# Kernel optimization log

Hardware: AMD Instinct MI355X
Metric: run time of the kernel (lower is better)

## Reference

```python
import jax, jax.numpy as jnp
import numpy as np

NV, NC, E, H, L = 100_000, 420_000, 630_000, 128, 8
ALPHA, THETA = 0.1, 0.5


def _seg_mean(msgs, dst, n_dst):
    # mean aggregation over destination segments (PyG SAGEConv default)
    s = jax.ops.segment_sum(msgs, dst, num_segments=n_dst)
    cnt = jax.ops.segment_sum(jnp.ones((dst.shape[0], 1), msgs.dtype), dst, num_segments=n_dst)
    return s / jnp.maximum(cnt, 1.0)


def _sage(x_src, x_dst, src, dst, n_dst, Wl, bl, Wr):
    # SAGEConv: lin_l(mean_{j in N(i)} x_j) + lin_r(x_i); lin_r has no bias
    agg = _seg_mean(x_src[src], dst, n_dst)
    return agg @ Wl + bl + x_dst @ Wr


def setup_inputs() -> dict:
    key = jax.random.key(0)
    ks = jax.random.split(key, 40)
    k = iter(range(40))
    rn = lambda shape, s=0.05: jax.random.normal(ks[next(k)], shape, jnp.float32) * s
    inp = {}
    inp['x_variable'] = jax.random.normal(ks[next(k)], (NV, 4), jnp.float32)
    inp['x_clause'] = jax.random.normal(ks[next(k)], (NC, 1), jnp.float32)
    src_p = jax.random.randint(ks[next(k)], (E,), 0, NV)
    dst_p = jax.random.randint(ks[next(k)], (E,), 0, NC)
    src_n = jax.random.randint(ks[next(k)], (E,), 0, NV)
    dst_n = jax.random.randint(ks[next(k)], (E,), 0, NC)
    inp['edge_pos'] = jnp.stack([src_p, dst_p])  # variable -> clause
    inp['edge_neg'] = jnp.stack([src_n, dst_n])
    inp['W_vemb'] = rn((4, H)); inp['b_vemb'] = rn((H,))
    inp['W_cemb'] = rn((1, H)); inp['b_cemb'] = rn((H,))
    for tag in ('pos', 'neg', 'rpos', 'rneg'):
        inp[f'Wl_{tag}'] = rn((L, H, H)); inp[f'bl_{tag}'] = rn((L, H))
        inp[f'Wr_{tag}'] = rn((L, H, H))
    inp['Wv'] = rn((L, H, H)); inp['bv'] = rn((L, H))
    inp['W_fin'] = rn((H, 1)); inp['b_fin'] = rn((1,))
    return inp


def reference(x_variable, x_clause, edge_pos, edge_neg,
              W_vemb, b_vemb, W_cemb, b_cemb,
              Wl_pos, bl_pos, Wr_pos, Wl_neg, bl_neg, Wr_neg,
              Wl_rpos, bl_rpos, Wr_rpos, Wl_rneg, bl_rneg, Wr_rneg,
              Wv, bv, W_fin, b_fin):
    v_h0 = jax.nn.relu(x_variable @ W_vemb + b_vemb)
    c_h0 = jax.nn.relu(x_clause @ W_cemb + b_cemb)
    v_h, c_h = v_h0, c_h0
    sp, dp = edge_pos[0], edge_pos[1]
    sn, dn = edge_neg[0], edge_neg[1]
    for i in range(L):
        v_old = v_h
        # HeteroConv(aggr='sum'): clause gets pos_in + neg_in, variable gets rev_pos_in + rev_neg_in
        c_new = (_sage(v_h, c_h, sp, dp, NC, Wl_pos[i], bl_pos[i], Wr_pos[i]) +
                 _sage(v_h, c_h, sn, dn, NC, Wl_neg[i], bl_neg[i], Wr_neg[i]))
        v_new = (_sage(c_h, v_h, dp, sp, NV, Wl_rpos[i], bl_rpos[i], Wr_rpos[i]) +
                 _sage(c_h, v_h, dn, sn, NV, Wl_rneg[i], bl_rneg[i], Wr_rneg[i]))
        v_h = (1.0 - ALPHA) * v_new + ALPHA * v_h0
        c_h = (1.0 - ALPHA) * c_new + ALPHA * c_h0
        beta = float(np.log(THETA / (i + 1) + 1.0))
        v_h = (1.0 - beta) * v_h + beta * (v_h @ Wv[i] + bv[i])
        v_h = v_h + v_old  # use_inter_layer_res=True
        v_h, c_h = jax.nn.relu(v_h), jax.nn.relu(c_h)
    return v_h @ W_fin + b_fin
```

## Files before the change

### kernel.cpp

```cpp
#include <hip/hip_runtime.h>
#include <math.h>

#define NVV 100000
#define NCC 420000
#define EE  630000
#define HH  128
#define LL  8

typedef unsigned int uint;
typedef unsigned short ushort;
typedef __attribute__((ext_vector_type(8))) short bf16x8;
typedef __attribute__((ext_vector_type(4))) float f32x4;

#define MFMA16(a,b,c) __builtin_amdgcn_mfma_f32_16x16x32_bf16(a,b,c,0,0,0)
#define SW(r,k) (((r)<<7) + ((k) ^ (((r)&7)<<3)))

__device__ inline float bf2f(uint u){ return __uint_as_float(u << 16); }
__device__ inline uint  f2bf(float f){
  uint b = __float_as_uint(f);
  return (b + 0x7FFFu + ((b >> 16) & 1u)) >> 16;
}
__device__ inline uint pack2(float a, float b){ return f2bf(a) | (f2bf(b) << 16); }
__device__ inline float4 relu4(float4 v){
  v.x = fmaxf(v.x, 0.f); v.y = fmaxf(v.y, 0.f);
  v.z = fmaxf(v.z, 0.f); v.w = fmaxf(v.w, 0.f);
  return v;
}

__global__ void k_sentinel(float* out, float v){
  if (blockIdx.x == 0 && threadIdx.x == 0) out[0] = v;
}

__device__ inline float4 vemb4(const float* __restrict__ xv, const float* __restrict__ W,
                               const float* __restrict__ b, int i, int h4){
  float x0 = xv[4*i+0], x1 = xv[4*i+1], x2 = xv[4*i+2], x3 = xv[4*i+3];
  float4 w0 = *(const float4*)(W + 0*HH + h4);
  float4 w1 = *(const float4*)(W + 1*HH + h4);
  float4 w2 = *(const float4*)(W + 2*HH + h4);
  float4 w3 = *(const float4*)(W + 3*HH + h4);
  float4 bb = *(const float4*)(b + h4);
  float4 r;
  r.x = fmaf(x0,w0.x, fmaf(x1,w1.x, fmaf(x2,w2.x, fmaf(x3,w3.x, bb.x))));
  r.y = fmaf(x0,w0.y, fmaf(x1,w1.y, fmaf(x2,w2.y, fmaf(x3,w3.y, bb.y))));
  r.z = fmaf(x0,w0.z, fmaf(x1,w1.z, fmaf(x2,w2.z, fmaf(x3,w3.z, bb.z))));
  r.w = fmaf(x0,w0.w, fmaf(x1,w1.w, fmaf(x2,w2.w, fmaf(x3,w3.w, bb.w))));
  return r;
}

__global__ void k_embed_v(const float* __restrict__ xv, const float* __restrict__ W,
                          const float* __restrict__ b, float* __restrict__ out){
  int tid = blockIdx.x * 256 + threadIdx.x;
  int i = tid >> 5;
  if (i >= NVV) return;
  int h4 = (tid & 31) << 2;
  *(float4*)(out + (size_t)i*HH + h4) = relu4(vemb4(xv, W, b, i, h4));
}

__global__ void k_embed_c(const float* __restrict__ xc, const float* __restrict__ W,
                          const float* __restrict__ b, uint* __restrict__ out){
  int tid = blockIdx.x * 256 + threadIdx.x;
  int i = tid >> 5;
  if (i >= NCC) return;
  int c2 = tid & 31;
  int h4 = c2 << 2;
  float x0 = xc[i];
  float4 w = *(const float4*)(W + h4);
  float4 bb = *(const float4*)(b + h4);
  float4 r;
  r.x = fmaxf(fmaf(x0, w.x, bb.x), 0.f);
  r.y = fmaxf(fmaf(x0, w.y, bb.y), 0.f);
  r.z = fmaxf(fmaf(x0, w.z, bb.z), 0.f);
  r.w = fmaxf(fmaf(x0, w.w, bb.w), 0.f);
  uint2 o; o.x = pack2(r.x, r.y); o.y = pack2(r.z, r.w);
  *(uint2*)(out + (size_t)i*64 + c2*2) = o;
}

__global__ void k_prep(const float* __restrict__ Wl_pos, const float* __restrict__ Wl_neg,
                       const float* __restrict__ Wl_rpos, const float* __restrict__ Wl_rneg,
                       const float* __restrict__ Wv, const float* __restrict__ Wr_pos,
                       const float* __restrict__ Wr_neg, const float* __restrict__ Wr_rpos,
                       const float* __restrict__ Wr_rneg, ushort* __restrict__ wt){
  int tid = blockIdx.x * 256 + threadIdx.x;
  int n4 = tid & 31, k = (tid >> 5) & 127, l = (tid >> 12) & 7, m = tid >> 15;
  const float* s1; const float* s2 = nullptr;
  switch (m){
    case 0: s1 = Wl_pos;  break;
    case 1: s1 = Wl_neg;  break;
    case 2: s1 = Wl_rpos; break;
    case 3: s1 = Wl_rneg; break;
    case 4: s1 = Wv;      break;
    case 5: s1 = Wr_pos;  s2 = Wr_neg;  break;
    default: s1 = Wr_rpos; s2 = Wr_rneg; break;
  }
  size_t o = (size_t)l*16384 + (size_t)k*128 + n4*4;
  float4 w = *(const float4*)(s1 + o);
  if (s2){
    float4 w2 = *(const float4*)(s2 + o);
    w.x += w2.x; w.y += w2.y; w.z += w2.z; w.w += w2.w;
  }
  ushort* hi = wt + (size_t)((m*LL + l)*2    )*16384;
  ushort* lo = wt + (size_t)((m*LL + l)*2 + 1)*16384;
  float vv[4] = {w.x, w.y, w.z, w.w};
  #pragma unroll
  for (int e = 0; e < 4; ++e){
    int n = n4*4 + e;
    uint h = f2bf(vv[e]);
    float r = vv[e] - bf2f(h);
    hi[SW(n, k)] = (ushort)h;
    lo[SW(n, k)] = (ushort)f2bf(r);
  }
}

__global__ void k_counti(const int* __restrict__ d, int* cnt, int n){
  int i = blockIdx.x * 256 + threadIdx.x;
  if (i < n) atomicAdd(&cnt[d[i]], 1);
}

#define SCAN256(ts, t) \
  for (int off = 1; off < 256; off <<= 1){ \
    int _a = (t >= off) ? ts[t - off] : 0; \
    __syncthreads(); \
    ts[t] += _a; \
    __syncthreads(); \
  }

__global__ void k_scanb(const int* __restrict__ in, int* __restrict__ out,
                        int* __restrict__ part, int n){
  __shared__ int ts[256];
  int b = blockIdx.x, t = threadIdx.x;
  int base = b*1024 + t*4;
  int v0 = (base+0 < n) ? in[base+0] : 0;
  int v1 = (base+1 < n) ? in[base+1] : 0;
  int v2 = (base+2 < n) ? in[base+2] : 0;
  int v3 = (base+3 < n) ? in[base+3] : 0;
  int s1 = v0, s2 = s1+v1, s3 = s2+v2, tsum = s3+v3;
  ts[t] = tsum; __syncthreads();
  SCAN256(ts, t)
  int excl = ts[t] - tsum;
  if (base+0 < n) out[base+0] = excl;
  if (base+1 < n) out[base+1] = excl + s1;
  if (base+2 < n) out[base+2] = excl + s2;
  if (base+3 < n) out[base+3] = excl + s3;
  if (t == 255) part[b] = ts[255];
}

__global__ void k_scanp(int* p, int nb){
  __shared__ int ts[256];
  __shared__ int carry;
  int t = threadIdx.x;
  if (t == 0) carry = 0;
  __syncthreads();
  for (int c = 0; c*256 < nb; ++c){
    int i = c*256 + t;
    int v = (i < nb) ? p[i] : 0;
    ts[t] = v; __syncthreads();
    SCAN256(ts, t)
    int excl = ts[t] - v + carry;
    if (i < nb) p[i] = excl;
    int tot = ts[255];
    __syncthreads();
    if (t == 0) carry += tot;
    __syncthreads();
  }
}

__global__ void k_scana(int* out, const int* __restrict__ part, int n){
  int i = blockIdx.x * 256 + threadIdx.x;
  if (i < n) out[i] += part[i >> 10];
}

__global__ void k_fill(const int* __restrict__ dst, const int* __restrict__ pay,
                       int* cur, int* __restrict__ eo, int n){
  int i = blockIdx.x * 256 + threadIdx.x;
  if (i >= n) return;
  int p = atomicAdd(&cur[dst[i]], 1);
  eo[p] = pay[i];
}

__global__ void k_vgather(const uint* __restrict__ ch,
                          const int* __restrict__ ipp, const int* __restrict__ epp,
                          const int* __restrict__ ipn, const int* __restrict__ epn,
                          uint* __restrict__ Up, uint* __restrict__ Un){
  int g = blockIdx.x * 256 + threadIdx.x;
  int v = g >> 6, lane = g & 63;
  if (v >= NVV) return;
  int sp = v ? ipp[v-1] : 0, ePos = ipp[v];
  int sn = v ? ipn[v-1] : 0, eNeg = ipn[v];
  float p0 = 0.f, p1 = 0.f, n0 = 0.f, n1 = 0.f;
  int jp = sp, jn = sn;
  while (jp < ePos && jn < eNeg){
    uint up = ch[(size_t)epp[jp]*64 + lane];
    uint un = ch[(size_t)epn[jn]*64 + lane];
    p0 += bf2f(up & 0xFFFFu); p1 += bf2f(up >> 16);
    n0 += bf2f(un & 0xFFFFu); n1 += bf2f(un >> 16);
    ++jp; ++jn;
  }
  for (; jp < ePos; ++jp){
    uint up = ch[(size_t)epp[jp]*64 + lane];
    p0 += bf2f(up & 0xFFFFu); p1 += bf2f(up >> 16);
  }
  for (; jn < eNeg; ++jn){
    uint un = ch[(size_t)epn[jn]*64 + lane];
    n0 += bf2f(un & 0xFFFFu); n1 += bf2f(un >> 16);
  }
  float ivp = 1.f / fmaxf((float)(ePos - sp), 1.f);
  float ivn = 1.f / fmaxf((float)(eNeg - sn), 1.f);
  Up[(size_t)v*64 + lane] = pack2(p0*ivp, p1*ivp);
  Un[(size_t)v*64 + lane] = pack2(n0*ivn, n1*ivn);
}

__device__ inline void stA_bf16(const uint4* __restrict__ A, ushort* As, int m0, int M, int t){
  #pragma unroll
  for (int j = 0; j < 4; ++j){
    int idx = j*512 + t, r = idx >> 4, c = idx & 15;
    uint4 v = make_uint4(0,0,0,0);
    if (m0 + r < M) v = A[(size_t)(m0 + r)*16 + c];
    *(uint4*)(As + SW(r, c*8)) = v;
  }
}

__device__ inline void stA_f32(const float* __restrict__ A, ushort* As, int m0, int M, int t){
  const float4* A4 = (const float4*)A;
  #pragma unroll
  for (int j = 0; j < 8; ++j){
    int idx = j*512 + t, r = idx >> 5, c = idx & 31;
    float4 v = make_float4(0.f,0.f,0.f,0.f);
    if (m0 + r < M) v = A4[(size_t)(m0 + r)*32 + c];
    uint2 u; u.x = pack2(v.x, v.y); u.y = pack2(v.z, v.w);
    *(uint2*)(As + SW(r, c*4)) = u;
  }
}

__device__ inline void stB(const uint4* __restrict__ Bt, ushort* Bs, int t){
  #pragma unroll
  for (int j = 0; j < 4; ++j) ((uint4*)Bs)[j*512 + t] = Bt[j*512 + t];
}

__device__ inline void kloop(const ushort* As, const ushort* Bs, int wr, int wc,
                             int l15, int g, f32x4 acc[2][4]){
  #pragma unroll
  for (int kk = 0; kk < 4; ++kk){
    int kb = kk*32 + g*8;
    bf16x8 a0 = *(const bf16x8*)(As + SW(wr*32 + l15,      kb));
    bf16x8 a1 = *(const bf16x8*)(As + SW(wr*32 + 16 + l15, kb));
    #pragma unroll
    for (int ni = 0; ni < 4; ++ni){
      int n = wc*64 + ni*16 + l15;
      bf16x8 b = *(const bf16x8*)(Bs + SW(n, kb));
      acc[0][ni] = MFMA16(a0, b, acc[0][ni]);
      acc[1][ni] = MFMA16(a1, b, acc[1][ni]);
    }
  }
}

__device__ inline void accStoreF(float* ldsF, f32x4 acc[2][4], int wr, int wc, int l15, int g){
  #pragma unroll
  for (int mi = 0; mi < 2; ++mi)
    #pragma unroll
    for (int ni = 0; ni < 4; ++ni)
      #pragma unroll
      for (int j = 0; j < 4; ++j)
        ldsF[(wr*32 + mi*16 + g*4 + j)*128 + wc*64 + ni*16 + l15] = acc[mi][ni][j];
}

__device__ inline void accStoreFsw(float* ldsF, f32x4 acc[2][4], int wr, int wc, int l15, int g){
  #pragma unroll
  for (int mi = 0; mi < 2; ++mi)
    #pragma unroll
    for (int ni = 0; ni < 4; ++ni)
      #pragma unroll
      for (int j = 0; j < 4; ++j){
        int r = wr*32 + mi*16 + g*4 + j;
        int c = wc*64 + ni*16 + l15;
        ldsF[r*128 + (((c >> 2) ^ (r & 31)) << 2) + (c & 3)] = acc[mi][ni][j];
      }
}

__device__ inline void accStoreBf(ushort* dst, f32x4 acc[2][4], int wr, int wc, int l15, int g){
  #pragma unroll
  for (int mi = 0; mi < 2; ++mi)
    #pragma unroll
    for (int ni = 0; ni < 4; ++ni)
      #pragma unroll
      for (int j = 0; j < 4; ++j)
        dst[(wr*32 + mi*16 + g*4 + j)*128 + wc*64 + ni*16 + l15] =
            (ushort)f2bf(acc[mi][ni][j]);
}

#define MMHEAD \
  __shared__ ushort lds[32768]; \
  ushort* As = lds; ushort* Bs = lds + 16384; \
  float* accumF = (float*)lds; \
  int t = threadIdx.x, m0 = blockIdx.x * 128; \
  int w = t >> 6, l = t & 63, wr = w >> 1, wc = w & 1, l15 = l & 15, g = l >> 4; \
  const f32x4 zz = {0.f, 0.f, 0.f, 0.f}; \
  (void)accumF;

#define ZACC(A) { \
  _Pragma("unroll") for (int mi_ = 0; mi_ < 2; ++mi_) \
    _Pragma("unroll") for (int ni_ = 0; ni_ < 4; ++ni_) A[mi_][ni_] = zz; }

__global__ __launch_bounds__(512) void k_fused_v(
    const uint4* __restrict__ AggP, const uint4* __restrict__ AggN,
    const uint4* __restrict__ Bph, const uint4* __restrict__ Bpl,
    const uint4* __restrict__ Bnh, const uint4* __restrict__ Bnl,
    const uint4* __restrict__ Bfh, const uint4* __restrict__ Bfl,
    const uint4* __restrict__ Byph, const uint4* __restrict__ Bypl,
    const uint4* __restrict__ Bynh, const uint4* __restrict__ Bynl,
    const uint4* __restrict__ Bvh, const uint4* __restrict__ Bvl,
    const float* __restrict__ xv, const float* __restrict__ Wve, const float* __restrict__ bve,
    const float* __restrict__ blp, const float* __restrict__ bln, const float* __restrict__ bvv,
    float omb, float beta,
    uint4* __restrict__ Yp, uint4* __restrict__ Yn, float* vh, int M){
  MMHEAD
  f32x4 accM[2][4], accP[2][4], accN[2][4];
  ZACC(accM) ZACC(accP) ZACC(accN)

  stA_bf16(AggP, As, m0, M, t); stB(Bph, Bs, t); __syncthreads();
  kloop(As, Bs, wr, wc, l15, g, accM); __syncthreads();
  stB(Bpl, Bs, t); __syncthreads();
  kloop(As, Bs, wr, wc, l15, g, accM); __syncthreads();
  stA_bf16(AggN, As, m0, M, t); stB(Bnh, Bs, t); __syncthreads();
  kloop(As, Bs, wr, wc, l15, g, accM); __syncthreads();
  stB(Bnl, Bs, t); __syncthreads();
  kloop(As, Bs, wr, wc, l15, g, accM); __syncthreads();
  stA_f32(vh, As, m0, M, t); stB(Bfh, Bs, t); __syncthreads();
  kloop(As, Bs, wr, wc, l15, g, accM); __syncthreads();
  stB(Bfl, Bs, t); __syncthreads();
  kloop(As, Bs, wr, wc, l15, g, accM); __syncthreads();
  stB(Byph, Bs, t); __syncthreads();
  kloop(As, Bs, wr, wc, l15, g, accP); __syncthreads();
  stB(Bypl, Bs, t); __syncthreads();
  kloop(As, Bs, wr, wc, l15, g, accP); __syncthreads();
  stB(Bynh, Bs, t); __syncthreads();
  kloop(As, Bs, wr, wc, l15, g, accN); __syncthreads();
  stB(Bynl, Bs, t); __syncthreads();
  kloop(As, Bs, wr, wc, l15, g, accN); __syncthreads();

  accStoreBf(lds,         accP, wr, wc, l15, g);
  accStoreBf(lds + 16384, accN, wr, wc, l15, g);
  __syncthreads();
  #pragma unroll
  for (int j = 0; j < 4; ++j){
    int idx = j*512 + t, r = idx >> 4, c = idx & 15;
    if (m0 + r < M){
      Yp[(size_t)(m0 + r)*16 + c] = ((const uint4*)lds)[idx];
      Yn[(size_t)(m0 + r)*16 + c] = ((const uint4*)(lds + 16384))[idx];
    }
  }
  __syncthreads();

  accStoreF(accumF, accM, wr, wc, l15, g);
  __syncthreads();
  float4 vreg[8];
  #pragma unroll
  for (int j = 0; j < 8; ++j){
    int idx = j*512 + t, r = idx >> 5, c4 = idx & 31;
    int row = m0 + r;
    float4 o = make_float4(0.f,0.f,0.f,0.f);
    if (row < M){
      float4 a4 = ((const float4*)accumF)[r*32 + c4];
      float4 bp = ((const float4*)blp)[c4];
      float4 bn = ((const float4*)bln)[c4];
      float4 h = relu4(vemb4(xv, Wve, bve, row, c4*4));
      o.x = 0.9f*(a4.x + bp.x + bn.x) + 0.1f*h.x;
      o.y = 0.9f*(a4.y + bp.y + bn.y) + 0.1f*h.y;
      o.z = 0.9f*(a4.z + bp.z + bn.z) + 0.1f*h.z;
      o.w = 0.9f*(a4.w + bp.w + bn.w) + 0.1f*h.w;
    }
    vreg[j] = o;
  }
  __syncthreads();
  #pragma unroll
  for (int j = 0; j < 8; ++j){
    int idx = j*512 + t, r = idx >> 5, c4 = idx & 31;
    uint2 u; u.x = pack2(vreg[j].x, vreg[j].y); u.y = pack2(vreg[j].z, vreg[j].w);
    *(uint2*)(As + SW(r, c4*4)) = u;
  }
  f32x4 accT[2][4];
  ZACC(accT)
  stB(Bvh, Bs, t); __syncthreads();
  kloop(As, Bs, wr, wc, l15, g, accT); __syncthreads();
  stB(Bvl, Bs, t); __syncthreads();
  kloop(As, Bs, wr, wc, l15, g, accT);

  #pragma unroll
  for (int mi = 0; mi < 2; ++mi)
    #pragma unroll
    for (int ni = 0; ni < 4; ++ni)
      #pragma unroll
      for (int j = 0; j < 4; ++j){
        int lr  = wr*32 + mi*16 + g*4 + j;
        int col = wc*64 + ni*16 + l15;
        int grow = m0 + lr;
        if (grow < M){
          float vm = bf2f((uint)As[SW(lr, col)]);
          float vo = vh[(size_t)grow*HH + col];
          float o  = fmaxf(omb*vm + beta*(accT[mi][ni][j] + bvv[col]) + vo, 0.f);
          vh[(size_t)grow*HH + col] = o;
        }
      }
}

__device__ inline void acc_yrow(float4 ga[8], uint4 u0, uint4 u1, uint4 u2, uint4 u3, float sc){
  uint4 uu[4] = {u0, u1, u2, u3};
  #pragma unroll
  for (int m = 0; m < 4; ++m){
    uint4 u = uu[m];
    ga[2*m].x   = fmaf(bf2f(u.x & 0xFFFFu), sc, ga[2*m].x);
    ga[2*m].y   = fmaf(bf2f(u.x >> 16),     sc, ga[2*m].y);
    ga[2*m].z   = fmaf(bf2f(u.y & 0xFFFFu), sc, ga[2*m].z);
    ga[2*m].w   = fmaf(bf2f(u.y >> 16),     sc, ga[2*m].w);
    ga[2*m+1].x = fmaf(bf2f(u.z & 0xFFFFu), sc, ga[2*m+1].x);
    ga[2*m+1].y = fmaf(bf2f(u.z >> 16),     sc, ga[2*m+1].y);
    ga[2*m+1].z = fmaf(bf2f(u.w & 0xFFFFu), sc, ga[2*m+1].z);
    ga[2*m+1].w = fmaf(bf2f(u.w >> 16),     sc, ga[2*m+1].w);
  }
}

__global__ __launch_bounds__(512) void k_mm_c(const uint4* ch,
    const uint4* __restrict__ Bh, const uint4* __restrict__ Bl,
    const int* __restrict__ ipp, const int* __restrict__ ecp,
    const int* __restrict__ ipn, const int* __restrict__ ecn,
    const uint4* __restrict__ Yp, const uint4* __restrict__ Yn,
    const float* __restrict__ xc, const float* __restrict__ Wc, const float* __restrict__ bc,
    const float* __restrict__ blp, const float* __restrict__ bln,
    uint2* chout){
  MMHEAD
  f32x4 acc[2][4];
  ZACC(acc)
  stA_bf16(ch, As, m0, NCC, t); stB(Bh, Bs, t); __syncthreads();
  kloop(As, Bs, wr, wc, l15, g, acc); __syncthreads();
  stB(Bl, Bs, t); __syncthreads();
  kloop(As, Bs, wr, wc, l15, g, acc); __syncthreads();
  accStoreFsw(accumF, acc, wr, wc, l15, g);
  __syncthreads();

  int r = t >> 2, q = t & 3, row = m0 + r;
  if (row >= NCC) return;
  float4 ga[8];
  #pragma unroll
  for (int m = 0; m < 8; ++m) ga[m] = make_float4(0.f,0.f,0.f,0.f);
  int sp = row ? ipp[row-1] : 0, ePos = ipp[row];
  int sn = row ? ipn[row-1] : 0, eNeg = ipn[row];
  float invp = 1.f / fmaxf((float)(ePos - sp), 1.f);
  float invn = 1.f / fmaxf((float)(eNeg - sn), 1.f);
  int jp = sp, jn = sn;
  while (jp < ePos && jn < eNeg){
    const uint4* yp = Yp + (size_t)ecp[jp]*16 + q*4;
    const uint4* yn = Yn + (size_t)ecn[jn]*16 + q*4;
    uint4 a0 = yp[0], a1 = yp[1], a2 = yp[2], a3 = yp[3];
    uint4 b0 = yn[0], b1 = yn[1], b2 = yn[2], b3 = yn[3];
    acc_yrow(ga, a0, a1, a2, a3, invp);
    acc_yrow(ga, b0, b1, b2, b3, invn);
    ++jp; ++jn;
  }
  while (jp < ePos){
    const uint4* yp = Yp + (size_t)ecp[jp]*16 + q*4;
    acc_yrow(ga, yp[0], yp[1], yp[2], yp[3], invp);
    ++jp;
  }
  while (jn < eNeg){
    const uint4* yn = Yn + (size_t)ecn[jn]*16 + q*4;
    acc_yrow(ga, yn[0], yn[1], yn[2], yn[3], invn);
    ++jn;
  }
  float xcv = xc[row];
  #pragma unroll
  for (int m = 0; m < 8; ++m){
    int gi = q*8 + m;
    float4 res = ((const float4*)accumF)[r*32 + (gi ^ (r & 31))];
    float4 wc4 = ((const float4*)Wc)[gi];
    float4 bcv = ((const float4*)bc)[gi];
    float4 bp  = ((const float4*)blp)[gi];
    float4 bn  = ((const float4*)bln)[gi];
    float4 h;
    h.x = fmaxf(fmaf(xcv, wc4.x, bcv.x), 0.f);
    h.y = fmaxf(fmaf(xcv, wc4.y, bcv.y), 0.f);
    h.z = fmaxf(fmaf(xcv, wc4.z, bcv.z), 0.f);
    h.w = fmaxf(fmaf(xcv, wc4.w, bcv.w), 0.f);
    float4 o;
    o.x = fmaxf(0.9f*(ga[m].x + res.x + bp.x + bn.x) + 0.1f*h.x, 0.f);
    o.y = fmaxf(0.9f*(ga[m].y + res.y + bp.y + bn.y) + 0.1f*h.y, 0.f);
    o.z = fmaxf(0.9f*(ga[m].z + res.z + bp.z + bn.z) + 0.1f*h.z, 0.f);
    o.w = fmaxf(0.9f*(ga[m].w + res.w + bp.w + bn.w) + 0.1f*h.w, 0.f);
    uint2 u2; u2.x = pack2(o.x, o.y); u2.y = pack2(o.z, o.w);
    chout[(size_t)row*32 + gi] = u2;
  }
}

__global__ void k_final(const float* __restrict__ vh, const float* __restrict__ wf,
                        const float* __restrict__ bf, float* __restrict__ out){
  int wid = (blockIdx.x * 256 + threadIdx.x) >> 6;
  if (wid >= NVV) return;
  int lane = threadIdx.x & 63;
  float2 a = *(const float2*)(vh + (size_t)wid*HH + lane*2);
  float2 w = *(const float2*)(wf + lane*2);
  float s = a.x*w.x + a.y*w.y;
  #pragma unroll
  for (int off = 32; off > 0; off >>= 1) s += __shfl_down(s, off);
  if (lane == 0) out[wid] = s + bf[0];
}

extern "C" void kernel_launch(void* const* d_in, const int* in_sizes, int n_in,
                              void* d_out, int out_size, void* d_ws, size_t ws_size,
                              hipStream_t stream) {
  const float* xv  = (const float*)d_in[0];
  const float* xc  = (const float*)d_in[1];
  const int*   ep  = (const int*)d_in[2];
  const int*   en  = (const int*)d_in[3];
  const float* Wve = (const float*)d_in[4];
  const float* bve = (const float*)d_in[5];
  const float* Wce = (const float*)d_in[6];
  const float* bce = (const float*)d_in[7];
  const float* Wl_pos  = (const float*)d_in[8];
  const float* bl_pos  = (const float*)d_in[9];
  const float* Wr_pos  = (const float*)d_in[10];
  const float* Wl_neg  = (const float*)d_in[11];
  const float* bl_neg  = (const float*)d_in[12];
  const float* Wr_neg  = (const float*)d_in[13];
  const float* Wl_rpos = (const float*)d_in[14];
  const float* bl_rpos = (const float*)d_in[15];
  const float* Wr_rpos = (const float*)d_in[16];
  const float* Wl_rneg = (const float*)d_in[17];
  const float* bl_rneg = (const float*)d_in[18];
  const float* Wr_rneg = (const float*)d_in[19];
  const float* Wv  = (const float*)d_in[20];
  const float* bv  = (const float*)d_in[21];
  const float* Wf  = (const float*)d_in[22];
  const float* bf  = (const float*)d_in[23];
  float* out = (float*)d_out;

  size_t off = 0;
  auto alloc = [&](size_t bytes) -> void* {
    void* p = (char*)d_ws + off;
    off = (off + bytes + 255) & ~(size_t)255;
    return p;
  };
  uint*   c_h  = (uint*)  alloc((size_t)NCC*64*sizeof(uint));
  float*  v_h  = (float*) alloc((size_t)NVV*HH*sizeof(float));
  uint*   U1   = (uint*)  alloc((size_t)NVV*64*sizeof(uint));
  uint*   U2   = (uint*)  alloc((size_t)NVV*64*sizeof(uint));
  ushort* wt   = (ushort*)alloc((size_t)7*LL*2*16384*sizeof(ushort));
  int*   ipc_p = (int*)  alloc((size_t)NCC*sizeof(int));
  int*   ec_p  = (int*)  alloc((size_t)EE*sizeof(int));
  int*   ipc_n = (int*)  alloc((size_t)NCC*sizeof(int));
  int*   ec_n  = (int*)  alloc((size_t)EE*sizeof(int));
  int*   ipv_p = (int*)  alloc((size_t)NVV*sizeof(int));
  int*   ev_p  = (int*)  alloc((size_t)EE*sizeof(int));
  int*   ipv_n = (int*)  alloc((size_t)NVV*sizeof(int));
  int*   ev_n  = (int*)  alloc((size_t)EE*sizeof(int));
  int*   part  = (int*)  alloc(4096);
  if (off > ws_size){
    k_sentinel<<<1, 64, 0, stream>>>(out, (float)(ws_size >> 20));
    return;
  }

  const int TB = 256;
  const int gE  = (EE + TB-1)/TB;
  const int gV  = (NVV*32 + TB-1)/TB;
  const int gC  = (NCC*32 + TB-1)/TB;
  const int gGv = (NVV + 127)/128;
  const int gGc = (NCC + 127)/128;
  const int gWd = (NVV*64 + TB-1)/TB;

  auto wp = [&](int m, int l, int h) -> const uint4* {
    return (const uint4*)(wt + (size_t)((m*LL + l)*2 + h)*16384);
  };

  auto build = [&](const int* dst, const int* pay, int nd, int* ip, int* eo){
    hipMemsetAsync(ip, 0, (size_t)nd*sizeof(int), stream);
    k_counti<<<gE, TB, 0, stream>>>(dst, ip, EE);
    int nb = (nd + 1023)/1024;
    k_scanb<<<nb, TB, 0, stream>>>(ip, ip, part, nd);
    k_scanp<<<1, TB, 0, stream>>>(part, nb);
    k_scana<<<(nd + TB-1)/TB, TB, 0, stream>>>(ip, part, nd);
    k_fill<<<gE, TB, 0, stream>>>(dst, pay, ip, eo, EE);
  };
  build(ep + EE, ep,      NCC, ipc_p, ec_p);
  build(en + EE, en,      NCC, ipc_n, ec_n);
  build(ep,      ep + EE, NVV, ipv_p, ev_p);
  build(en,      en + EE, NVV, ipv_n, ev_n);

  k_prep<<<(7*LL*128*32)/TB, TB, 0, stream>>>(Wl_pos, Wl_neg, Wl_rpos, Wl_rneg, Wv,
                                              Wr_pos, Wr_neg, Wr_rpos, Wr_rneg, wt);

  k_embed_v<<<gV, TB, 0, stream>>>(xv, Wve, bve, v_h);
  k_embed_c<<<gC, TB, 0, stream>>>(xc, Wce, bce, c_h);

  for (int l = 0; l < LL; ++l){
    const size_t bo = (size_t)l*HH;
    double beta_d = log(0.5/(double)(l+1) + 1.0);

    k_vgather<<<gWd, TB, 0, stream>>>(c_h, ipv_p, ev_p, ipv_n, ev_n, U1, U2);
    k_fused_v<<<gGv, 512, 0, stream>>>((const uint4*)U1, (const uint4*)U2,
                                       wp(2,l,0), wp(2,l,1), wp(3,l,0), wp(3,l,1),
                                       wp(6,l,0), wp(6,l,1),
                                       wp(0,l,0), wp(0,l,1), wp(1,l,0), wp(1,l,1),
                                       wp(4,l,0), wp(4,l,1),
                                       xv, Wve, bve, bl_rpos + bo, bl_rneg + bo, bv + bo,
                                       (float)(1.0 - beta_d), (float)beta_d,
                                       (uint4*)U1, (uint4*)U2, v_h, NVV);
    k_mm_c<<<gGc, 512, 0, stream>>>((const uint4*)c_h, wp(5,l,0), wp(5,l,1),
                                    ipc_p, ec_p, ipc_n, ec_n,
                                    (const uint4*)U1, (const uint4*)U2,
                                    xc, Wce, bce, bl_pos + bo, bl_neg + bo,
                                    (uint2*)c_h);
  }

  k_final<<<gWd, TB, 0, stream>>>(v_h, Wf, bf, out);
}
```

Before: 3.794 ms.

## Coalesce v_h epilogue via LDS staging and remap clause gather threads

The variable-update epilogue now stages the MFMA accumulator through LDS in two halves, then reads and writes v_h with row-contiguous float4 accesses instead of scattered per-element accesses. In the clause kernel, each row's gather is now handled by 16 threads doing one uint4 load each, over four passes of 32 rows, instead of 4 threads doing four uint4 loads each. Positive and negative sums are kept separately and scaled once at the end, which removes per-edge multiplies. Both changes target uncoalesced global traffic, at the cost of extra barriers and less per-thread memory-level parallelism in the gather.

```diff
diff --git a/kernel.cpp b/kernel.cpp
--- a/kernel.cpp
+++ b/kernel.cpp
@@ -384,38 +384,47 @@
   stB(Bvl, Bs, t); __syncthreads();
   kloop(As, Bs, wr, wc, l15, g, accT);
 
-  #pragma unroll
-  for (int mi = 0; mi < 2; ++mi)
+  float* ldsH = (float*)Bs;
+  #pragma unroll
+  for (int half = 0; half < 2; ++half){
+    __syncthreads();
+    if ((wr >> 1) == half){
+      int rbase = (wr & 1)*32;
+      #pragma unroll
+      for (int mi = 0; mi < 2; ++mi)
+        #pragma unroll
+        for (int ni = 0; ni < 4; ++ni)
+          #pragma unroll
+          for (int j = 0; j < 4; ++j)
+            ldsH[(rbase + mi*16 + g*4 + j)*128 + wc*64 + ni*16 + l15] = accT[mi][ni][j];
+    }
+    __syncthreads();
     #pragma unroll
-    for (int ni = 0; ni < 4; ++ni)
-      #pragma unroll
-      for (int j = 0; j < 4; ++j){
-        int lr  = wr*32 + mi*16 + g*4 + j;
-        int col = wc*64 + ni*16 + l15;
-        int grow = m0 + lr;
-        if (grow < M){
-          float vm = bf2f((uint)As[SW(lr, col)]);
-          float vo = vh[(size_t)grow*HH + col];
-          float o  = fmaxf(omb*vm + beta*(accT[mi][ni][j] + bvv[col]) + vo, 0.f);
-          vh[(size_t)grow*HH + col] = o;
-        }
-      }
-}
-
-__device__ inline void acc_yrow(float4 ga[8], uint4 u0, uint4 u1, uint4 u2, uint4 u3, float sc){
-  uint4 uu[4] = {u0, u1, u2, u3};
-  #pragma unroll
-  for (int m = 0; m < 4; ++m){
-    uint4 u = uu[m];
-    ga[2*m].x   = fmaf(bf2f(u.x & 0xFFFFu), sc, ga[2*m].x);
-    ga[2*m].y   = fmaf(bf2f(u.x >> 16),     sc, ga[2*m].y);
-    ga[2*m].z   = fmaf(bf2f(u.y & 0xFFFFu), sc, ga[2*m].z);
-    ga[2*m].w   = fmaf(bf2f(u.y >> 16),     sc, ga[2*m].w);
-    ga[2*m+1].x = fmaf(bf2f(u.z & 0xFFFFu), sc, ga[2*m+1].x);
-    ga[2*m+1].y = fmaf(bf2f(u.z >> 16),     sc, ga[2*m+1].y);
-    ga[2*m+1].z = fmaf(bf2f(u.w & 0xFFFFu), sc, ga[2*m+1].z);
-    ga[2*m+1].w = fmaf(bf2f(u.w >> 16),     sc, ga[2*m+1].w);
-  }
+    for (int j = 0; j < 4; ++j){
+      int idx = j*512 + t, r2 = idx >> 5, c4 = idx & 31;
+      int row = m0 + half*64 + r2;
+      if (row >= M) continue;
+      float4 a4 = ((const float4*)ldsH)[r2*32 + c4];
+      uint2 um = *(const uint2*)(As + SW(half*64 + r2, c4*4));
+      float4 bb = ((const float4*)bvv)[c4];
+      float4 vo = *(const float4*)(vh + (size_t)row*HH + c4*4);
+      float m0f = bf2f(um.x & 0xFFFFu), m1f = bf2f(um.x >> 16);
+      float m2f = bf2f(um.y & 0xFFFFu), m3f = bf2f(um.y >> 16);
+      float4 o;
+      o.x = fmaxf(omb*m0f + beta*(a4.x + bb.x) + vo.x, 0.f);
+      o.y = fmaxf(omb*m1f + beta*(a4.y + bb.y) + vo.y, 0.f);
+      o.z = fmaxf(omb*m2f + beta*(a4.z + bb.z) + vo.z, 0.f);
+      o.w = fmaxf(omb*m3f + beta*(a4.w + bb.w) + vo.w, 0.f);
+      *(float4*)(vh + (size_t)row*HH + c4*4) = o;
+    }
+  }
+}
+
+__device__ inline void addrow8(float f[8], uint4 u){
+  f[0] += bf2f(u.x & 0xFFFFu); f[1] += bf2f(u.x >> 16);
+  f[2] += bf2f(u.y & 0xFFFFu); f[3] += bf2f(u.y >> 16);
+  f[4] += bf2f(u.z & 0xFFFFu); f[5] += bf2f(u.z >> 16);
+  f[6] += bf2f(u.w & 0xFFFFu); f[7] += bf2f(u.w >> 16);
 }
 
 __global__ __launch_bounds__(512) void k_mm_c(const uint4* ch,
@@ -425,7 +434,7 @@
     const uint4* __restrict__ Yp, const uint4* __restrict__ Yn,
     const float* __restrict__ xc, const float* __restrict__ Wc, const float* __restrict__ bc,
     const float* __restrict__ blp, const float* __restrict__ bln,
-    uint2* chout){
+    uint4* chout){
   MMHEAD
   f32x4 acc[2][4];
   ZACC(acc)
@@ -436,56 +445,54 @@
   accStoreFsw(accumF, acc, wr, wc, l15, g);
   __syncthreads();
 
-  int r = t >> 2, q = t & 3, row = m0 + r;
-  if (row >= NCC) return;
-  float4 ga[8];
-  #pragma unroll
-  for (int m = 0; m < 8; ++m) ga[m] = make_float4(0.f,0.f,0.f,0.f);
-  int sp = row ? ipp[row-1] : 0, ePos = ipp[row];
-  int sn = row ? ipn[row-1] : 0, eNeg = ipn[row];
-  float invp = 1.f / fmaxf((float)(ePos - sp), 1.f);
-  float invn = 1.f / fmaxf((float)(eNeg - sn), 1.f);
-  int jp = sp, jn = sn;
-  while (jp < ePos && jn < eNeg){
-    const uint4* yp = Yp + (size_t)ecp[jp]*16 + q*4;
-    const uint4* yn = Yn + (size_t)ecn[jn]*16 + q*4;
-    uint4 a0 = yp[0], a1 = yp[1], a2 = yp[2], a3 = yp[3];
-    uint4 b0 = yn[0], b1 = yn[1], b2 = yn[2], b3 = yn[3];
-    acc_yrow(ga, a0, a1, a2, a3, invp);
-    acc_yrow(ga, b0, b1, b2, b3, invn);
-    ++jp; ++jn;
-  }
-  while (jp < ePos){
-    const uint4* yp = Yp + (size_t)ecp[jp]*16 + q*4;
-    acc_yrow(ga, yp[0], yp[1], yp[2], yp[3], invp);
-    ++jp;
-  }
-  while (jn < eNeg){
-    const uint4* yn = Yn + (size_t)ecn[jn]*16 + q*4;
-    acc_yrow(ga, yn[0], yn[1], yn[2], yn[3], invn);
-    ++jn;
-  }
-  float xcv = xc[row];
-  #pragma unroll
-  for (int m = 0; m < 8; ++m){
-    int gi = q*8 + m;
-    float4 res = ((const float4*)accumF)[r*32 + (gi ^ (r & 31))];
-    float4 wc4 = ((const float4*)Wc)[gi];
-    float4 bcv = ((const float4*)bc)[gi];
-    float4 bp  = ((const float4*)blp)[gi];
-    float4 bn  = ((const float4*)bln)[gi];
-    float4 h;
-    h.x = fmaxf(fmaf(xcv, wc4.x, bcv.x), 0.f);
-    h.y = fmaxf(fmaf(xcv, wc4.y, bcv.y), 0.f);
-    h.z = fmaxf(fmaf(xcv, wc4.z, bcv.z), 0.f);
-    h.w = fmaxf(fmaf(xcv, wc4.w, bcv.w), 0.f);
-    float4 o;
-    o.x = fmaxf(0.9f*(ga[m].x + res.x + bp.x + bn.x) + 0.1f*h.x, 0.f);
-    o.y = fmaxf(0.9f*(ga[m].y + res.y + bp.y + bn.y) + 0.1f*h.y, 0.f);
-    o.z = fmaxf(0.9f*(ga[m].z + res.z + bp.z + bn.z) + 0.1f*h.z, 0.f);
-    o.w = fmaxf(0.9f*(ga[m].w + res.w + bp.w + bn.w) + 0.1f*h.w, 0.f);
-    uint2 u2; u2.x = pack2(o.x, o.y); u2.y = pack2(o.z, o.w);
-    chout[(size_t)row*32 + gi] = u2;
+  int c16 = t & 15;
+  int rg  = t >> 4;
+  #pragma unroll
+  for (int pass = 0; pass < 4; ++pass){
+    int r = pass*32 + rg;
+    int row = m0 + r;
+    if (row >= NCC) continue;
+    float fp[8] = {0,0,0,0,0,0,0,0};
+    float fn[8] = {0,0,0,0,0,0,0,0};
+    int sp = row ? ipp[row-1] : 0, ePos = ipp[row];
+    int sn = row ? ipn[row-1] : 0, eNeg = ipn[row];
+    int jp = sp, jn = sn;
+    while (jp < ePos && jn < eNeg){
+      uint4 up = Yp[(size_t)ecp[jp]*16 + c16];
+      uint4 un = Yn[(size_t)ecn[jn]*16 + c16];
+      addrow8(fp, up);
+      addrow8(fn, un);
+      ++jp; ++jn;
+    }
+    for (; jp < ePos; ++jp) addrow8(fp, Yp[(size_t)ecp[jp]*16 + c16]);
+    for (; jn < eNeg; ++jn) addrow8(fn, Yn[(size_t)ecn[jn]*16 + c16]);
+    float invp = 1.f / fmaxf((float)(ePos - sp), 1.f);
+    float invn = 1.f / fmaxf((float)(eNeg - sn), 1.f);
+
+    int gi0 = c16*2, gi1 = gi0 + 1;
+    float4 res0 = ((const float4*)accumF)[r*32 + (gi0 ^ (r & 31))];
+    float4 res1 = ((const float4*)accumF)[r*32 + (gi1 ^ (r & 31))];
+    float4 wc0 = ((const float4*)Wc)[gi0],  wc1 = ((const float4*)Wc)[gi1];
+    float4 bc0 = ((const float4*)bc)[gi0],  bc1 = ((const float4*)bc)[gi1];
+    float4 bp0 = ((const float4*)blp)[gi0], bp1 = ((const float4*)blp)[gi1];
+    float4 bn0 = ((const float4*)bln)[gi0], bn1 = ((const float4*)bln)[gi1];
+    float xcv = xc[row];
+    float res[8] = {res0.x,res0.y,res0.z,res0.w, res1.x,res1.y,res1.z,res1.w};
+    float wcv[8] = {wc0.x,wc0.y,wc0.z,wc0.w, wc1.x,wc1.y,wc1.z,wc1.w};
+    float bcv[8] = {bc0.x,bc0.y,bc0.z,bc0.w, bc1.x,bc1.y,bc1.z,bc1.w};
+    float bpv[8] = {bp0.x,bp0.y,bp0.z,bp0.w, bp1.x,bp1.y,bp1.z,bp1.w};
+    float bnv[8] = {bn0.x,bn0.y,bn0.z,bn0.w, bn1.x,bn1.y,bn1.z,bn1.w};
+    float o[8];
+    #pragma unroll
+    for (int k = 0; k < 8; ++k){
+      float h = fmaxf(fmaf(xcv, wcv[k], bcv[k]), 0.f);
+      float m = fmaf(fp[k], invp, fn[k]*invn);
+      o[k] = fmaxf(0.9f*(m + res[k] + bpv[k] + bnv[k]) + 0.1f*h, 0.f);
+    }
+    uint4 u;
+    u.x = pack2(o[0], o[1]); u.y = pack2(o[2], o[3]);
+    u.z = pack2(o[4], o[5]); u.w = pack2(o[6], o[7]);
+    chout[(size_t)row*16 + c16] = u;
   }
 }
 
@@ -605,7 +612,7 @@
                                     ipc_p, ec_p, ipc_n, ec_n,
                                     (const uint4*)U1, (const uint4*)U2,
                                     xc, Wce, bce, bl_pos + bo, bl_neg + bo,
-                                    (uint2*)c_h);
+                                    (uint4*)c_h);
   }
 
   k_final<<<gWd, TB, 0, stream>>>(v_h, Wf, bf, out);
```

After: 3.517 ms. 1.08x faster.
